# Performance work log

Measured on AMD Instinct MI355X. Metric: run time of the kernel, lower is better.

## Reference

```python
import jax, jax.numpy as jnp
import numpy as np

N_NODES = 100000
N_EDGES = 1600000
N_FEAT = 7
HIDDEN = [128, 128, 128]
N_CLASS = 5
N_GRAPHS = 8


def _glorot(key, shape):
    fan_in, fan_out = shape[0], shape[1]
    lim = (6.0 / (fan_in + fan_out)) ** 0.5
    return jax.random.uniform(key, shape, jnp.float32, -lim, lim)


def setup_inputs() -> dict:
    key = jax.random.key(0)
    ks = jax.random.split(key, 16)
    x = jax.random.normal(ks[0], (N_NODES, N_FEAT), jnp.float32)
    edge_index = jax.random.randint(ks[1], (2, N_EDGES), 0, N_NODES, jnp.int64 if jax.config.jax_enable_x64 else jnp.int32)
    edge_attr = jax.random.normal(ks[2], (N_EDGES, 1), jnp.float32)
    batch = jnp.sort(jax.random.randint(ks[3], (N_NODES,), 0, N_GRAPHS))
    dims_in = [N_FEAT, HIDDEN[0], HIDDEN[1]]
    params = {}
    for i in range(3):
        params[f"We{i+1}"] = _glorot(ks[4 + 2 * i], (1, dims_in[i]))
        params[f"be{i+1}"] = jnp.zeros((dims_in[i],), jnp.float32)
        params[f"W{i+1}"] = _glorot(ks[5 + 2 * i], (dims_in[i], HIDDEN[i]))
        params[f"b{i+1}"] = jnp.zeros((HIDDEN[i],), jnp.float32)
    params["Wlin"] = _glorot(ks[10], (HIDDEN[2], N_CLASS))
    params["blin"] = jnp.zeros((N_CLASS,), jnp.float32)
    return dict(x=x, edge_index=edge_index, edge_attr=edge_attr, batch=batch, **params)


def _gine(x, src, dst, edge_attr, We, be, W, b, eps=0.0):
    # edge_attr [E,1] -> [E,in]; message = relu(x_j + lin(edge_attr)); scatter-add to target
    e = edge_attr @ We + be
    m = jax.nn.relu(x[src] + e)                      # [E, in]
    agg = jax.ops.segment_sum(m, dst, num_segments=N_NODES)
    h = agg + (1.0 + eps) * x                        # [N, in]
    return jax.nn.relu(h @ W + b)                    # nn = Linear + ReLU


def reference(x, edge_index, edge_attr, batch,
              We1, be1, W1, b1, We2, be2, W2, b2, We3, be3, W3, b3,
              Wlin, blin):
    src, dst = edge_index[0], edge_index[1]
    h = _gine(x, src, dst, edge_attr, We1, be1, W1, b1)
    h = jax.nn.relu(h)  # extra .relu() in forward (idempotent, kept for fidelity)
    h = _gine(h, src, dst, edge_attr, We2, be2, W2, b2)
    h = jax.nn.relu(h)
    h = _gine(h, src, dst, edge_attr, We3, be3, W3, b3)
    # global mean pool over graphs
    sums = jax.ops.segment_sum(h, batch, num_segments=N_GRAPHS)
    cnts = jax.ops.segment_sum(jnp.ones((N_NODES, 1), h.dtype), batch, num_segments=N_GRAPHS)
    pooled = sums / jnp.maximum(cnts, 1.0)
    # dropout is identity in eval mode
    return pooled @ Wlin + blin
```

## Files before the change

kernel.cpp:

```cpp
#include <hip/hip_runtime.h>
#include <hip/hip_bf16.h>

#define N_NODES 100000
#define N_EDGES 1600000
#define N_FEAT 7
#define HID 128
#define N_CLASS 5
#define N_GRAPHS 8
#define NPB 16
#define TLP 136
#define TLP1 40
#define NBKT 196
#define BKT_SHIFT 9
#define TILE 4096

typedef __hip_bfloat16 bf16;
typedef __attribute__((ext_vector_type(8))) short short8;
typedef __attribute__((ext_vector_type(4))) float f32x4;


__global__ __launch_bounds__(256) void bucket_hist(const int* __restrict__ dst,
                                                   int* __restrict__ gcnt) {
    __shared__ int l[NBKT];
    int tid = threadIdx.x;
    for (int i = tid; i < NBKT; i += 256) l[i] = 0;
    __syncthreads();
    int e0 = blockIdx.x * TILE;
    int ne = N_EDGES - e0; if (ne > TILE) ne = TILE;
    for (int t = tid; t < ne; t += 256)
        atomicAdd(&l[dst[e0 + t] >> BKT_SHIFT], 1);
    __syncthreads();
    for (int i = tid; i < NBKT; i += 256)
        if (l[i]) atomicAdd(&gcnt[i], l[i]);
}

__global__ __launch_bounds__(256) void scan_buckets(const int* __restrict__ gcnt,
                                                    int* __restrict__ bstart,
                                                    int* __restrict__ bcur,
                                                    int* __restrict__ rowptr,
                                                    float* __restrict__ pool) {
    __shared__ int s[256];
    int tid = threadIdx.x;
    int v = (tid < NBKT) ? gcnt[tid] : 0;
    s[tid] = v;
    __syncthreads();
    for (int o = 1; o < 256; o <<= 1) {
        int u = (tid >= o) ? s[tid - o] : 0;
        __syncthreads();
        s[tid] += u;
        __syncthreads();
    }
    if (tid < NBKT) { bstart[tid] = s[tid] - v; bcur[tid] = s[tid] - v; }
    if (tid == 0) rowptr[N_NODES] = N_EDGES;
    for (int i = tid; i < N_GRAPHS * HID + N_GRAPHS; i += 256) pool[i] = 0.f;
}

__global__ __launch_bounds__(256) void partition_kernel(
        const int* __restrict__ src, const int* __restrict__ dst,
        const float* __restrict__ ea, int* __restrict__ bcur,
        int2* __restrict__ tmp2, int* __restrict__ tmpd) {
    __shared__ int lsrc[TILE], lea[TILE], ldst[TILE];
    __shared__ int cnt[NBKT], gbase[NBKT];
    __shared__ int off[256];
    int tid = threadIdx.x;
    int e0 = blockIdx.x * TILE;
    int nedge = N_EDGES - e0; if (nedge > TILE) nedge = TILE;

    for (int bkt = tid; bkt < NBKT; bkt += 256) cnt[bkt] = 0;
    __syncthreads();
    for (int t = tid; t < nedge; t += 256)
        atomicAdd(&cnt[dst[e0 + t] >> BKT_SHIFT], 1);
    __syncthreads();
    off[tid] = (tid < NBKT) ? cnt[tid] : 0;
    __syncthreads();
    for (int o = 1; o < 256; o <<= 1) {
        int u = (tid >= o) ? off[tid - o] : 0;
        __syncthreads();
        off[tid] += u;
        __syncthreads();
    }
    if (tid < NBKT) {
        off[tid] -= cnt[tid];
        gbase[tid] = atomicAdd(&bcur[tid], cnt[tid]);
    }
    __syncthreads();
    if (tid < NBKT) cnt[tid] = 0;
    __syncthreads();
    for (int t = tid; t < nedge; t += 256) {
        int d = dst[e0 + t];
        int bkt = d >> BKT_SHIFT;
        int sp = off[bkt] + atomicAdd(&cnt[bkt], 1);
        lsrc[sp] = src[e0 + t];
        lea[sp] = __float_as_int(ea[e0 + t]);
        ldst[sp] = d;
    }
    __syncthreads();
    for (int t = tid; t < nedge; t += 256) {
        int d = ldst[t];
        int bkt = d >> BKT_SHIFT;
        int gi = gbase[bkt] + (t - off[bkt]);
        tmp2[gi] = make_int2(lsrc[t], lea[t]);
        tmpd[gi] = d;
    }
}

__global__ __launch_bounds__(512) void bucket_sort(
        const int2* __restrict__ tmp2, const int* __restrict__ tmpd,
        const int* __restrict__ bstart, const int* __restrict__ gcnt,
        int* __restrict__ rowptr, int2* __restrict__ csr) {
    __shared__ int s[512];
    __shared__ int lcur[512];
    int tid = threadIdx.x;
    int b = blockIdx.x;
    int nb0 = b << BKT_SHIFT;
    int r0 = bstart[b];
    int r1 = r0 + gcnt[b];
    s[tid] = 0;
    __syncthreads();
    for (int i = r0 + tid; i < r1; i += 512)
        atomicAdd(&s[tmpd[i] - nb0], 1);
    __syncthreads();
    int v = s[tid];
    for (int o = 1; o < 512; o <<= 1) {
        int u = (tid >= o) ? s[tid - o] : 0;
        __syncthreads();
        s[tid] += u;
        __syncthreads();
    }
    int excl = s[tid] - v;
    lcur[tid] = excl;
    int n = nb0 + tid;
    if (n < N_NODES) rowptr[n] = r0 + excl;
    __syncthreads();
    for (int i = r0 + tid; i < r1; i += 512) {
        int d = tmpd[i];
        int p = r0 + atomicAdd(&lcur[d - nb0], 1);
        csr[p] = tmp2[i];
    }
}


__device__ __forceinline__ void pack_w_body(const float* W, bf16* Wp, int t) {
    int l = t & 63;
    int kk = (t >> 6) & 3;
    int jt = t >> 8;
    int kbase = kk * 32 + (l >> 4) * 8;
    int j = jt * 16 + (l & 15);
#pragma unroll
    for (int q = 0; q < 8; ++q)
        Wp[t * 8 + q] = __float2bfloat16(W[(kbase + q) * HID + j]);
}

__global__ __launch_bounds__(256) void pack_all(
        const float* __restrict__ W2, const float* __restrict__ W3,
        const float* __restrict__ W1, const float* __restrict__ x,
        bf16* __restrict__ Wp2, bf16* __restrict__ Wp3,
        bf16* __restrict__ Wp1, bf16* __restrict__ xp) {
    int bid = blockIdx.x, tid = threadIdx.x;
    if (bid < 8) {
        pack_w_body(W2, Wp2, bid * 256 + tid);
    } else if (bid < 16) {
        pack_w_body(W3, Wp3, (bid - 8) * 256 + tid);
    } else if (bid < 18) {
        int t = (bid - 16) * 256 + tid;
        if (t < 512) {
            int l = t & 63;
            int jt = t >> 6;
            int j = jt * 16 + (l & 15);
#pragma unroll
            for (int q = 0; q < 8; ++q) {
                int k = (l >> 4) * 8 + q;
                Wp1[t * 8 + q] = __float2bfloat16(k < N_FEAT ? W1[k * HID + j] : 0.f);
            }
        }
    } else {
        int n = (bid - 18) * 256 + tid;
        if (n < N_NODES) {
            unsigned short pk[8];
#pragma unroll
            for (int k = 0; k < N_FEAT; ++k) {
                bf16 h = __float2bfloat16(x[n * N_FEAT + k]);
                pk[k] = *(unsigned short*)&h;
            }
            pk[7] = 0;
            *(uint4*)&xp[(size_t)n * 8] = *(const uint4*)pk;
        }
    }
}

__global__ __launch_bounds__(256) void layer1_fused(
        const bf16* __restrict__ xp, const int2* __restrict__ csr,
        const int* __restrict__ rowptr, const float* __restrict__ We,
        const float* __restrict__ be, const bf16* __restrict__ Wp1,
        const float* __restrict__ b, bf16* __restrict__ hout) {
    __shared__ __align__(16) unsigned short tl[NPB][TLP1];
    int tid = threadIdx.x;
    int wave = tid >> 6;
    int lane = tid & 63;
    int sub = lane >> 4;
    int l = lane & 15;
    int n0 = blockIdx.x * NPB;

    for (int i = tid; i < NPB * TLP1; i += 256) ((unsigned short*)tl)[i] = 0;

    float we[N_FEAT], bee[N_FEAT], p[N_FEAT];
#pragma unroll
    for (int k = 0; k < N_FEAT; ++k) { we[k] = We[k]; bee[k] = be[k]; p[k] = 0.f; }
    __syncthreads();

    const uint4* xp4 = (const uint4*)xp;
    int m = wave * 4 + sub;
    int n = n0 + m;
    int r0 = rowptr[n], r1 = rowptr[n + 1];
    for (int i = r0 + l; i < r1; i += 16) {
        int2 sa = csr[i];
        float a = __int_as_float(sa.y);
        uint4 rv = xp4[sa.x];
#pragma unroll
        for (int p_ = 0; p_ < 4; ++p_) {
            unsigned u = ((const unsigned*)&rv)[p_];
            float f0 = __uint_as_float(u << 16);
            float m0 = f0 + a * we[2 * p_] + bee[2 * p_];
            p[2 * p_] += m0 > 0.f ? m0 : 0.f;
            if (2 * p_ + 1 < N_FEAT) {
                float f1 = __uint_as_float(u & 0xffff0000u);
                float m1 = f1 + a * we[2 * p_ + 1] + bee[2 * p_ + 1];
                p[2 * p_ + 1] += m1 > 0.f ? m1 : 0.f;
            }
        }
    }
#pragma unroll
    for (int off = 8; off >= 1; off >>= 1)
#pragma unroll
        for (int k = 0; k < N_FEAT; ++k)
            p[k] += __shfl_xor(p[k], off, 16);
    if (l == 0) {
        uint4 sv = xp4[n];
#pragma unroll
        for (int k = 0; k < N_FEAT; ++k) {
            unsigned u = ((const unsigned*)&sv)[k >> 1];
            float fs = __uint_as_float((k & 1) ? (u & 0xffff0000u) : (u << 16));
            bf16 hb = __float2bfloat16(p[k] + fs);
            tl[m][k] = *(unsigned short*)&hb;
        }
    }
    __syncthreads();

    int c = lane & 15;
    int kq = lane >> 4;
    int jt0 = wave * 2, jt1 = jt0 + 1;
    f32x4 d0 = {0.f, 0.f, 0.f, 0.f}, d1 = {0.f, 0.f, 0.f, 0.f};
    const short8* wp = (const short8*)Wp1;
    short8 aF = *(const short8*)&tl[c][kq * 8];
    short8 b0 = wp[jt0 * 64 + lane];
    short8 b1 = wp[jt1 * 64 + lane];
    d0 = __builtin_amdgcn_mfma_f32_16x16x32_bf16(aF, b0, d0, 0, 0, 0);
    d1 = __builtin_amdgcn_mfma_f32_16x16x32_bf16(aF, b1, d1, 0, 0, 0);
    float bv0 = b[jt0 * 16 + c];
    float bv1 = b[jt1 * 16 + c];
#pragma unroll
    for (int i = 0; i < 4; ++i) {
        int mm = kq * 4 + i;
        size_t base = (size_t)(n0 + mm) * HID;
        float v0 = d0[i] + bv0;
        float v1 = d1[i] + bv1;
        hout[base + jt0 * 16 + c] = __float2bfloat16(v0 > 0.f ? v0 : 0.f);
        hout[base + jt1 * 16 + c] = __float2bfloat16(v1 > 0.f ? v1 : 0.f);
    }
}

__global__ __launch_bounds__(256) void hidden_layer(
        const bf16* __restrict__ hin, const int2* __restrict__ csr,
        const int* __restrict__ rowptr, const float* __restrict__ We,
        const float* __restrict__ be, const bf16* __restrict__ Wp,
        const float* __restrict__ b, bf16* __restrict__ hout) {
    __shared__ __align__(16) unsigned short tl[NPB][TLP];
    int tid = threadIdx.x;
    int wave = tid >> 6;
    int lane = tid & 63;
    int el = lane >> 4;
    int fc = lane & 15;
    int n0 = blockIdx.x * NPB;

    float we8[8], be8[8];
#pragma unroll
    for (int q = 0; q < 8; ++q) {
        we8[q] = We[fc * 8 + q];
        be8[q] = be[fc * 8 + q];
    }

    const uint4* hin4 = (const uint4*)hin;

    for (int loc = 0; loc < 4; ++loc) {
        int m = wave * 4 + loc;
        int n = n0 + m;
        int r0 = rowptr[n], r1 = rowptr[n + 1];
        float acc[8];
#pragma unroll
        for (int q = 0; q < 8; ++q) acc[q] = 0.f;
#pragma unroll 2
        for (int i = r0 + el; i < r1; i += 4) {
            int2 sa = csr[i];
            int s = sa.x;
            float a = __int_as_float(sa.y);
            uint4 rv = hin4[(size_t)s * 16 + fc];
#pragma unroll
            for (int p = 0; p < 4; ++p) {
                unsigned u = ((const unsigned*)&rv)[p];
                float f0 = __uint_as_float(u << 16);
                float f1 = __uint_as_float(u & 0xffff0000u);
                float m0 = f0 + a * we8[2 * p] + be8[2 * p];
                float m1 = f1 + a * we8[2 * p + 1] + be8[2 * p + 1];
                acc[2 * p]     += m0 > 0.f ? m0 : 0.f;
                acc[2 * p + 1] += m1 > 0.f ? m1 : 0.f;
            }
        }
#pragma unroll
        for (int q = 0; q < 8; ++q) {
            acc[q] += __shfl_xor(acc[q], 16, 64);
            acc[q] += __shfl_xor(acc[q], 32, 64);
        }
        if (el == 0) {
            uint4 sv = hin4[(size_t)n * 16 + fc];
            unsigned short pk[8];
#pragma unroll
            for (int p = 0; p < 4; ++p) {
                unsigned u = ((const unsigned*)&sv)[p];
                float v0 = acc[2 * p]     + __uint_as_float(u << 16);
                float v1 = acc[2 * p + 1] + __uint_as_float(u & 0xffff0000u);
                bf16 h0 = __float2bfloat16(v0);
                bf16 h1 = __float2bfloat16(v1);
                pk[2 * p]     = *(unsigned short*)&h0;
                pk[2 * p + 1] = *(unsigned short*)&h1;
            }
            *(uint4*)&tl[m][fc * 8] = *(const uint4*)pk;
        }
    }
    __syncthreads();

    int c = lane & 15;
    int kq = lane >> 4;
    int jt0 = wave * 2, jt1 = jt0 + 1;
    f32x4 d0 = {0.f, 0.f, 0.f, 0.f}, d1 = {0.f, 0.f, 0.f, 0.f};
    const short8* wp = (const short8*)Wp;
#pragma unroll
    for (int kk = 0; kk < 4; ++kk) {
        short8 a  = *(const short8*)&tl[c][kk * 32 + kq * 8];
        short8 b0 = wp[(jt0 * 4 + kk) * 64 + lane];
        short8 b1 = wp[(jt1 * 4 + kk) * 64 + lane];
        d0 = __builtin_amdgcn_mfma_f32_16x16x32_bf16(a, b0, d0, 0, 0, 0);
        d1 = __builtin_amdgcn_mfma_f32_16x16x32_bf16(a, b1, d1, 0, 0, 0);
    }
    float bv0 = b[jt0 * 16 + c];
    float bv1 = b[jt1 * 16 + c];
#pragma unroll
    for (int i = 0; i < 4; ++i) {
        int m = kq * 4 + i;
        size_t base = (size_t)(n0 + m) * HID;
        float v0 = d0[i] + bv0;
        float v1 = d1[i] + bv1;
        hout[base + jt0 * 16 + c] = __float2bfloat16(v0 > 0.f ? v0 : 0.f);
        hout[base + jt1 * 16 + c] = __float2bfloat16(v1 > 0.f ? v1 : 0.f);
    }
}


__global__ void pool_kernel(const bf16* __restrict__ h, const int* __restrict__ batch,
                            float* __restrict__ pool, float* __restrict__ cnt) {
    int n0 = blockIdx.x * 64;
    int j = threadIdx.x;
    int nend = n0 + 64;
    if (nend > N_NODES) nend = N_NODES;
    if (n0 >= N_NODES) return;
    float sum = 0.f;
    int curg = batch[n0];
    int runstart = n0;
    for (int n = n0; n < nend; ++n) {
        int g = batch[n];
        if (g != curg) {
            atomicAdd(&pool[curg * HID + j], sum);
            if (j == 0) atomicAdd(&cnt[curg], (float)(n - runstart));
            sum = 0.f;
            curg = g;
            runstart = n;
        }
        sum += __bfloat162float(h[(size_t)n * HID + j]);
    }
    atomicAdd(&pool[curg * HID + j], sum);
    if (j == 0) atomicAdd(&cnt[curg], (float)(nend - runstart));
}

__global__ void final_kernel(const float* __restrict__ pool, const float* __restrict__ cnt,
                             const float* __restrict__ Wlin, const float* __restrict__ blin,
                             float* __restrict__ out) {
    int idx = threadIdx.x;
    if (idx >= N_GRAPHS * N_CLASS) return;
    int g = idx / N_CLASS, c = idx % N_CLASS;
    float invc = 1.f / fmaxf(cnt[g], 1.f);
    float acc = blin[c];
    for (int j = 0; j < HID; ++j) acc += pool[g * HID + j] * invc * Wlin[j * N_CLASS + c];
    out[idx] = acc;
}

extern "C" void kernel_launch(void* const* d_in, const int* in_sizes, int n_in,
                              void* d_out, int out_size, void* d_ws, size_t ws_size,
                              hipStream_t stream) {
    const float* x    = (const float*)d_in[0];
    const int*   ei   = (const int*)d_in[1];
    const float* ea   = (const float*)d_in[2];
    const int*   batch= (const int*)d_in[3];
    const float* We1  = (const float*)d_in[4];
    const float* be1  = (const float*)d_in[5];
    const float* W1   = (const float*)d_in[6];
    const float* b1   = (const float*)d_in[7];
    const float* We2  = (const float*)d_in[8];
    const float* be2  = (const float*)d_in[9];
    const float* W2   = (const float*)d_in[10];
    const float* b2   = (const float*)d_in[11];
    const float* We3  = (const float*)d_in[12];
    const float* be3  = (const float*)d_in[13];
    const float* W3   = (const float*)d_in[14];
    const float* b3   = (const float*)d_in[15];
    const float* Wlin = (const float*)d_in[16];
    const float* blin = (const float*)d_in[17];

    const int* src = ei;
    const int* dst = ei + N_EDGES;

    char* w = (char*)d_ws;
    int2*  csr    = (int2*)w;                    w += sizeof(int2) * (size_t)N_EDGES;
    bf16*  Wp2    = (bf16*)w;                    w += sizeof(bf16) * 8 * 4 * 64 * 8;
    bf16*  Wp3    = (bf16*)w;                    w += sizeof(bf16) * 8 * 4 * 64 * 8;
    bf16*  Wp1    = (bf16*)w;                    w += sizeof(bf16) * 8 * 64 * 8;
    bf16*  xp     = (bf16*)w;                    w += sizeof(bf16) * (size_t)N_NODES * 8;
    bf16*  A      = (bf16*)w;                    w += sizeof(bf16) * (size_t)N_NODES * HID;
    bf16*  B      = (bf16*)w;                    w += sizeof(bf16) * (size_t)N_NODES * HID;
    float* pool   = (float*)w;                   w += sizeof(float) * N_GRAPHS * HID;
    float* cnt    = (float*)w;                   w += sizeof(float) * N_GRAPHS;
    int*   rowptr = (int*)w;                     w += sizeof(int) * (N_NODES + 1);
    int*   gcnt   = (int*)w;                     w += sizeof(int) * NBKT;
    int*   bstart = (int*)w;                     w += sizeof(int) * NBKT;
    int*   bcur   = (int*)w;                     w += sizeof(int) * NBKT;

    int2* tmp2 = (int2*)A;
    int*  tmpd = (int*)((char*)A + sizeof(int2) * (size_t)N_EDGES);

    hipMemsetAsync(gcnt, 0, sizeof(int) * NBKT, stream);
    bucket_hist<<<(N_EDGES + TILE - 1) / TILE, 256, 0, stream>>>(dst, gcnt);
    pack_all<<<18 + (N_NODES + 255) / 256, 256, 0, stream>>>(W2, W3, W1, x, Wp2, Wp3, Wp1, xp);
    scan_buckets<<<1, 256, 0, stream>>>(gcnt, bstart, bcur, rowptr, pool);
    partition_kernel<<<(N_EDGES + TILE - 1) / TILE, 256, 0, stream>>>(src, dst, ea, bcur, tmp2, tmpd);
    bucket_sort<<<NBKT, 512, 0, stream>>>(tmp2, tmpd, bstart, gcnt, rowptr, csr);

    layer1_fused<<<N_NODES / NPB, 256, 0, stream>>>(xp, csr, rowptr, We1, be1, Wp1, b1, A);

    hidden_layer<<<N_NODES / NPB, 256, 0, stream>>>(A, csr, rowptr, We2, be2, Wp2, b2, B);

    hidden_layer<<<N_NODES / NPB, 256, 0, stream>>>(B, csr, rowptr, We3, be3, Wp3, b3, A);

    pool_kernel<<<(N_NODES + 63) / 64, HID, 0, stream>>>(A, batch, pool, cnt);
    final_kernel<<<1, 64, 0, stream>>>(pool, cnt, Wlin, blin, (float*)d_out);
}
```

Measured before the change: 382.3 us.

## Fuse global mean pooling into last hidden layer via shared-memory accumulation

The third GINE layer no longer writes its bf16 output. It accumulates the ReLU outputs into per-graph sums in shared memory and then atomically adds them to the global pool. This removes the separate pool_kernel launch and the 25.6MB write and re-read of the final activations. The cost is extra LDS use in the template (a 4KB per-graph buffer, even for the non-pool instantiation), an LDS zeroing pass, LDS atomics, and global atomics from every one of the 6250 blocks. Sums also stay in fp32 instead of being rounded to bf16 first, and the pool now depends on the scan kernel having zeroed it before this kernel runs.

New measurement: 412.0 us. 1.08x slower.

```diff
diff --git a/kernel.cpp b/kernel.cpp
--- a/kernel.cpp
+++ b/kernel.cpp
@@ -269,18 +269,28 @@
     }
 }
 
+template<int POOL>
 __global__ __launch_bounds__(256) void hidden_layer(
         const bf16* __restrict__ hin, const int2* __restrict__ csr,
         const int* __restrict__ rowptr, const float* __restrict__ We,
         const float* __restrict__ be, const bf16* __restrict__ Wp,
-        const float* __restrict__ b, bf16* __restrict__ hout) {
+        const float* __restrict__ b, bf16* __restrict__ hout,
+        const int* __restrict__ batch, float* __restrict__ gpool,
+        float* __restrict__ gcnt) {
     __shared__ __align__(16) unsigned short tl[NPB][TLP];
+    __shared__ float pl[N_GRAPHS][HID];
+    __shared__ int bb[NPB];
     int tid = threadIdx.x;
     int wave = tid >> 6;
     int lane = tid & 63;
     int el = lane >> 4;
     int fc = lane & 15;
     int n0 = blockIdx.x * NPB;
+
+    if (POOL) {
+        for (int i = tid; i < N_GRAPHS * HID; i += 256) ((float*)pl)[i] = 0.f;
+        if (tid < NPB) bb[tid] = batch[n0 + tid];
+    }
 
     float we8[8], be8[8];
 #pragma unroll
@@ -356,39 +366,42 @@
 #pragma unroll
     for (int i = 0; i < 4; ++i) {
         int m = kq * 4 + i;
-        size_t base = (size_t)(n0 + m) * HID;
         float v0 = d0[i] + bv0;
         float v1 = d1[i] + bv1;
-        hout[base + jt0 * 16 + c] = __float2bfloat16(v0 > 0.f ? v0 : 0.f);
-        hout[base + jt1 * 16 + c] = __float2bfloat16(v1 > 0.f ? v1 : 0.f);
-    }
-}
-
-
-__global__ void pool_kernel(const bf16* __restrict__ h, const int* __restrict__ batch,
-                            float* __restrict__ pool, float* __restrict__ cnt) {
-    int n0 = blockIdx.x * 64;
-    int j = threadIdx.x;
-    int nend = n0 + 64;
-    if (nend > N_NODES) nend = N_NODES;
-    if (n0 >= N_NODES) return;
-    float sum = 0.f;
-    int curg = batch[n0];
-    int runstart = n0;
-    for (int n = n0; n < nend; ++n) {
-        int g = batch[n];
-        if (g != curg) {
-            atomicAdd(&pool[curg * HID + j], sum);
-            if (j == 0) atomicAdd(&cnt[curg], (float)(n - runstart));
-            sum = 0.f;
-            curg = g;
-            runstart = n;
-        }
-        sum += __bfloat162float(h[(size_t)n * HID + j]);
-    }
-    atomicAdd(&pool[curg * HID + j], sum);
-    if (j == 0) atomicAdd(&cnt[curg], (float)(nend - runstart));
-}
+        v0 = v0 > 0.f ? v0 : 0.f;
+        v1 = v1 > 0.f ? v1 : 0.f;
+        if (POOL) {
+            int g = bb[m];
+            atomicAdd(&pl[g][jt0 * 16 + c], v0);
+            atomicAdd(&pl[g][jt1 * 16 + c], v1);
+        } else {
+            size_t base = (size_t)(n0 + m) * HID;
+            hout[base + jt0 * 16 + c] = __float2bfloat16(v0);
+            hout[base + jt1 * 16 + c] = __float2bfloat16(v1);
+        }
+    }
+
+    if (POOL) {
+        __syncthreads();
+        int gmin = bb[0], gmax = bb[NPB - 1];
+        int j = tid & 127;
+        for (int g = gmin + (tid >> 7); g <= gmax; g += 2) {
+            float v = pl[g][j];
+            if (v != 0.f) atomicAdd(&gpool[g * HID + j], v);
+        }
+        if (tid == 0) {
+            int cg = bb[0], cc = 0;
+#pragma unroll
+            for (int i = 0; i < NPB; ++i) {
+                int g = bb[i];
+                if (g != cg) { atomicAdd(&gcnt[cg], (float)cc); cg = g; cc = 0; }
+                cc++;
+            }
+            atomicAdd(&gcnt[cg], (float)cc);
+        }
+    }
+}
+
 
 __global__ void final_kernel(const float* __restrict__ pool, const float* __restrict__ cnt,
                              const float* __restrict__ Wlin, const float* __restrict__ blin,
@@ -454,10 +467,11 @@
 
     layer1_fused<<<N_NODES / NPB, 256, 0, stream>>>(xp, csr, rowptr, We1, be1, Wp1, b1, A);
 
-    hidden_layer<<<N_NODES / NPB, 256, 0, stream>>>(A, csr, rowptr, We2, be2, Wp2, b2, B);
-
-    hidden_layer<<<N_NODES / NPB, 256, 0, stream>>>(B, csr, rowptr, We3, be3, Wp3, b3, A);
-
-    pool_kernel<<<(N_NODES + 63) / 64, HID, 0, stream>>>(A, batch, pool, cnt);
+    hidden_layer<0><<<N_NODES / NPB, 256, 0, stream>>>(A, csr, rowptr, We2, be2, Wp2, b2, B,
+                                                       batch, nullptr, nullptr);
+
+    hidden_layer<1><<<N_NODES / NPB, 256, 0, stream>>>(B, csr, rowptr, We3, be3, Wp3, b3, nullptr,
+                                                       batch, pool, cnt);
+
     final_kernel<<<1, 64, 0, stream>>>(pool, cnt, Wlin, blin, (float*)d_out);
 }
```
